# Kernel optimization log

Measured on AMD Instinct MI355X. Metric: run time of the kernel, lower is better.

Reference implementation:

```python
import jax, jax.numpy as jnp
import numpy as np

N_NODES = 50000
N_EDGES = 800000


def setup_inputs() -> dict:
    key = jax.random.key(0)
    ks = jax.random.split(key, 9)
    d, h, hd = 128, 4, 32
    s = 1.0 / np.sqrt(d)
    return {
        "x": jax.random.normal(ks[0], (N_NODES, d), jnp.float32),
        "edge_index": jax.random.randint(ks[1], (2, N_EDGES), 0, N_NODES, jnp.int32),
        "W0": jax.random.normal(ks[2], (d, d), jnp.float32) * s,
        "att_l0": jax.random.normal(ks[3], (h, hd), jnp.float32) * s,
        "att_r0": jax.random.normal(ks[4], (h, hd), jnp.float32) * s,
        "b0": jnp.zeros((d,), jnp.float32),
        "W1": jax.random.normal(ks[5], (d, d), jnp.float32) * s,
        "att_l1": jax.random.normal(ks[6], (h, hd), jnp.float32) * s,
        "att_r1": jax.random.normal(ks[7], (h, hd), jnp.float32) * s,
        "b1": jnp.zeros((hd,), jnp.float32),
    }


def _gat_layer(x, src, dst, W, att_l, att_r, bias, concat):
    # x: [N, F_in]; W: [H*D, F_in] (torch Linear layout); att_*: [H, D]
    n = x.shape[0]
    h, d = att_l.shape
    hx = (x @ W.T).reshape(n, h, d)                     # [N,H,D]
    al = jnp.einsum('nhd,hd->nh', hx, att_l)            # [N,H]
    ar = jnp.einsum('nhd,hd->nh', hx, att_r)
    att = al[src] + ar[dst]                             # [E,H]
    att = jax.nn.leaky_relu(att, negative_slope=0.2)
    # segment softmax over destination nodes
    m = jax.ops.segment_max(att, dst, num_segments=n)   # [N,H]
    att = jnp.exp(att - m[dst])
    ssum = jax.ops.segment_sum(att, dst, num_segments=n)
    att = att / (ssum[dst] + 1e-9)                      # [E,H]
    msgs = att[:, :, None] * hx[src]                    # [E,H,D]
    out = jax.ops.segment_sum(msgs, dst, num_segments=n)  # [N,H,D]
    if concat:
        out = out.reshape(n, h * d)
    else:
        out = out.mean(axis=1)
    return out + bias


def reference(x, edge_index, W0, att_l0, att_r0, b0, W1, att_l1, att_r1, b1):
    src, dst = edge_index[0], edge_index[1]
    x = _gat_layer(x, src, dst, W0, att_l0, att_r0, b0, concat=True)
    x = jax.nn.relu(x)  # dropout is identity in eval mode
    x = _gat_layer(x, src, dst, W1, att_l1, att_r1, b1, concat=False)
    return x
```

## Files before the change

### kernel.cpp

```cpp
#include <hip/hip_runtime.h>
#include <hip/hip_bf16.h>

#define H 4
#define D 32
#define F 128
#define MAXDEG 64
#define PF 16
#define NBUCK 256
#define BUCKW 196
#define CAP   4096

typedef __attribute__((ext_vector_type(8))) short bf16x8;
typedef __attribute__((ext_vector_type(4))) float f32x4;

__device__ __forceinline__ short f2bf(float v) {
    __hip_bfloat16 h = __float2bfloat16(v);
    return *reinterpret_cast<short*>(&h);
}
__device__ __forceinline__ float bf2f(short s) {
    __hip_bfloat16 h = *reinterpret_cast<__hip_bfloat16*>(&s);
    return __bfloat162float(h);
}

__device__ __forceinline__
void gemm_body(int bid, int nblocks, const float* __restrict__ X,
               const float* __restrict__ W, const float* __restrict__ attl,
               const float* __restrict__ attr, __hip_bfloat16* __restrict__ HXB,
               float* __restrict__ AL, float* __restrict__ AR, int ntiles) {
    const int wave = threadIdx.x >> 6;
    const int lane = threadIdx.x & 63;
    const int m    = lane & 15;
    const int q    = lane >> 4;
    const int q8   = q * 8;

    bf16x8 Bhi[2][4], Blo[2][4];
#pragma unroll
    for (int j = 0; j < 2; ++j) {
        const int fout = wave * 32 + j * 16 + m;
#pragma unroll
        for (int kc = 0; kc < 4; ++kc) {
            const float* wp = W + (size_t)fout * F + kc * 32 + q8;
            float4 w0 = *reinterpret_cast<const float4*>(wp);
            float4 w1 = *reinterpret_cast<const float4*>(wp + 4);
            float wv[8] = {w0.x, w0.y, w0.z, w0.w, w1.x, w1.y, w1.z, w1.w};
#pragma unroll
            for (int t = 0; t < 8; ++t) {
                short h = f2bf(wv[t]);
                Bhi[j][kc][t] = h;
                Blo[j][kc][t] = f2bf(wv[t] - bf2f(h));
            }
        }
    }
    const float alw0  = attl[wave * 32 + m];
    const float alw16 = attl[wave * 32 + 16 + m];
    const float arw0  = attr[wave * 32 + m];
    const float arw16 = attr[wave * 32 + 16 + m];

    for (int tile = bid; tile < ntiles; tile += nblocks) {
        const int node0 = tile * 16;
        bf16x8 Ahi[4], Alo[4];
        const float* xp = X + (size_t)(node0 + m) * F + q8;
#pragma unroll
        for (int kc = 0; kc < 4; ++kc) {
            float4 x0 = *reinterpret_cast<const float4*>(xp + kc * 32);
            float4 x1 = *reinterpret_cast<const float4*>(xp + kc * 32 + 4);
            float xv[8] = {x0.x, x0.y, x0.z, x0.w, x1.x, x1.y, x1.z, x1.w};
#pragma unroll
            for (int t = 0; t < 8; ++t) {
                short h = f2bf(xv[t]);
                Ahi[kc][t] = h;
                Alo[kc][t] = f2bf(xv[t] - bf2f(h));
            }
        }
        f32x4 acc0 = {0.f, 0.f, 0.f, 0.f};
        f32x4 acc1 = {0.f, 0.f, 0.f, 0.f};
#pragma unroll
        for (int kc = 0; kc < 4; ++kc) {
            acc0 = __builtin_amdgcn_mfma_f32_16x16x32_bf16(Ahi[kc], Bhi[0][kc], acc0, 0, 0, 0);
            acc1 = __builtin_amdgcn_mfma_f32_16x16x32_bf16(Ahi[kc], Bhi[1][kc], acc1, 0, 0, 0);
            acc0 = __builtin_amdgcn_mfma_f32_16x16x32_bf16(Ahi[kc], Blo[0][kc], acc0, 0, 0, 0);
            acc1 = __builtin_amdgcn_mfma_f32_16x16x32_bf16(Ahi[kc], Blo[1][kc], acc1, 0, 0, 0);
            acc0 = __builtin_amdgcn_mfma_f32_16x16x32_bf16(Alo[kc], Bhi[0][kc], acc0, 0, 0, 0);
            acc1 = __builtin_amdgcn_mfma_f32_16x16x32_bf16(Alo[kc], Bhi[1][kc], acc1, 0, 0, 0);
        }
        const int row0 = node0 + q * 4;
        const int col0 = wave * 32 + m;
#pragma unroll
        for (int r = 0; r < 4; ++r) {
            HXB[(size_t)(row0 + r) * F + col0]      = __float2bfloat16(acc0[r]);
            HXB[(size_t)(row0 + r) * F + col0 + 16] = __float2bfloat16(acc1[r]);
            float pal = acc0[r] * alw0 + acc1[r] * alw16;
            float par = acc0[r] * arw0 + acc1[r] * arw16;
#pragma unroll
            for (int o = 1; o < 16; o <<= 1) {
                pal += __shfl_xor(pal, o);
                par += __shfl_xor(par, o);
            }
            if (m == 0) {
                AL[(size_t)(row0 + r) * H + wave] = pal;
                AR[(size_t)(row0 + r) * H + wave] = par;
            }
        }
    }
}

__device__ __forceinline__
void wconv_body(const float* __restrict__ W1, __hip_bfloat16* __restrict__ W1hi,
                __hip_bfloat16* __restrict__ W1lo) {
    for (int i = threadIdx.x; i < F * F; i += 256) {
        float v = W1[i];
        short hi = f2bf(v);
        *reinterpret_cast<short*>(&W1hi[i]) = hi;
        *reinterpret_cast<short*>(&W1lo[i]) = f2bf(v - bf2f(hi));
    }
}

__device__ __forceinline__
void bucketA_body(int abid, int nablk, const int* __restrict__ ei, int E,
                  int* __restrict__ gcnt, unsigned int* __restrict__ buf) {
    __shared__ int lcnt[NBUCK];
    __shared__ int lpos[NBUCK];
    const int tid = threadIdx.x;
    lcnt[tid] = 0;
    __syncthreads();
    const int per = E / nablk;
    const int e0 = abid * per;
    const int e1 = (abid == nablk - 1) ? E : e0 + per;
    for (int e = e0 + tid; e < e1; e += 256)
        atomicAdd(&lcnt[ei[E + e] / BUCKW], 1);
    __syncthreads();
    if (lcnt[tid] > 0)
        lpos[tid] = atomicAdd(&gcnt[tid], lcnt[tid]);
    __syncthreads();
    for (int e = e0 + tid; e < e1; e += 256) {
        int src = ei[e];
        int dst = ei[E + e];
        int b = dst / BUCKW;
        int pos = atomicAdd(&lpos[b], 1);
        if (pos < CAP)
            buf[(size_t)b * CAP + pos] =
                (unsigned)src | ((unsigned)(dst - b * BUCKW) << 16);
    }
}

__global__ __launch_bounds__(256)
void k_pre(const float* __restrict__ X, const float* __restrict__ W0,
           const float* __restrict__ attl0, const float* __restrict__ attr0,
           __hip_bfloat16* __restrict__ HXB, float* __restrict__ AL,
           float* __restrict__ AR, int ntiles, int gemm_blocks,
           const float* __restrict__ W1, __hip_bfloat16* __restrict__ W1hi,
           __hip_bfloat16* __restrict__ W1lo,
           const int* __restrict__ ei, int E, int nablk,
           int* __restrict__ gcnt, unsigned int* __restrict__ buf) {
    const int bid = blockIdx.x;
    if (bid < gemm_blocks)
        gemm_body(bid, gemm_blocks, X, W0, attl0, attr0, HXB, AL, AR, ntiles);
    else if (bid == gemm_blocks)
        wconv_body(W1, W1hi, W1lo);
    else
        bucketA_body(bid - gemm_blocks - 1, nablk, ei, E, gcnt, buf);
}

__global__ __launch_bounds__(256)
void k_bucket(const unsigned int* __restrict__ buf, const int* __restrict__ gcnt,
              int* __restrict__ deg, unsigned short* __restrict__ ssrc2u, int N) {
    __shared__ int cnt[BUCKW];
    const int b = blockIdx.x;
    const int tid = threadIdx.x;
    if (tid < BUCKW) cnt[tid] = 0;
    __syncthreads();
    const int m = min(gcnt[b], CAP);
    for (int i = tid; i < m; i += 256) {
        unsigned rec = buf[(size_t)b * CAP + i];
        int src  = rec & 0xffff;
        int ldst = rec >> 16;
        int slot = atomicAdd(&cnt[ldst], 1);
        if (slot < MAXDEG)
            ssrc2u[(size_t)(b * BUCKW + ldst) * MAXDEG + slot] = (unsigned short)src;
    }
    __syncthreads();
    if (tid < BUCKW) {
        int node = b * BUCKW + tid;
        if (node < N) deg[node] = cnt[tid];
    }
}

__device__ __forceinline__
int stage_node(int g, int t, int n, const unsigned short* __restrict__ ssrc2u,
               const int* __restrict__ deg, const float* __restrict__ AL,
               const float4 ar4, int (*sidx)[MAXDEG], float (*sw)[MAXDEG][H]) {
    const int cnt  = min(deg[n], MAXDEG);
    const int rcnt = (cnt + PF - 1) & ~(PF - 1);
    if (t < rcnt) {
        if (t < cnt) {
            int s = ssrc2u[n * MAXDEG + t];
            sidx[g][t] = s;
            float4 al4 = *reinterpret_cast<const float4*>(AL + (size_t)s * H);
            float a0 = al4.x + ar4.x; a0 = a0 > 0.f ? a0 : 0.2f * a0;
            float a1 = al4.y + ar4.y; a1 = a1 > 0.f ? a1 : 0.2f * a1;
            float a2 = al4.z + ar4.z; a2 = a2 > 0.f ? a2 : 0.2f * a2;
            float a3 = al4.w + ar4.w; a3 = a3 > 0.f ? a3 : 0.2f * a3;
            sw[g][t][0] = __expf(a0);
            sw[g][t][1] = __expf(a1);
            sw[g][t][2] = __expf(a2);
            sw[g][t][3] = __expf(a3);
        } else {
            sidx[g][t] = 0;
            sw[g][t][0] = 0.f; sw[g][t][1] = 0.f; sw[g][t][2] = 0.f; sw[g][t][3] = 0.f;
        }
    }
    __builtin_amdgcn_wave_barrier();
    return rcnt;
}

__device__ __forceinline__
void gather_node(int g, int t, int h, int rcnt, const __hip_bfloat16* __restrict__ HXB,
                 const int (*sidx)[MAXDEG], const float (*sw)[MAXDEG][H],
                 float& accx, float& accy, float& wsum) {
    for (int base = 0; base < rcnt; base += PF) {
        __hip_bfloat162 v[PF];
#pragma unroll
        for (int j = 0; j < PF; ++j) {
            int s = sidx[g][base + j];
            v[j] = *reinterpret_cast<const __hip_bfloat162*>(HXB + (size_t)s * F + 2 * t);
        }
#pragma unroll
        for (int j = 0; j < PF; ++j) {
            float w = sw[g][base + j][h];
            float2 f = __bfloat1622float2(v[j]);
            accx += w * f.x;
            accy += w * f.y;
            wsum += w;
        }
    }
}

__global__ __launch_bounds__(256)
void k_aggr0(const unsigned short* __restrict__ ssrc2u, const int* __restrict__ deg,
             const float* __restrict__ AL, const float* __restrict__ AR,
             const __hip_bfloat16* __restrict__ HXB, const float* __restrict__ bias,
             float* __restrict__ out, int N) {
    __shared__ int   sidx[4][MAXDEG];
    __shared__ float sw[4][MAXDEG][H];
    const int g = threadIdx.x >> 6;
    const int t = threadIdx.x & 63;
    const int n = blockIdx.x * 4 + g;
    if (n >= N) return;
    const int h = t >> 4;
    const float4 ar4 = *reinterpret_cast<const float4*>(AR + (size_t)n * H);
    int rcnt = stage_node(g, t, n, ssrc2u, deg, AL, ar4, sidx, sw);
    float accx = 0.f, accy = 0.f, wsum = 0.f;
    gather_node(g, t, h, rcnt, HXB, sidx, sw, accx, accy, wsum);
    float inv = 1.f / (wsum + 1e-9f);
    float2 o;
    o.x = fmaxf(accx * inv + bias[2 * t], 0.f);
    o.y = fmaxf(accy * inv + bias[2 * t + 1], 0.f);
    *reinterpret_cast<float2*>(out + (size_t)n * F + 2 * t) = o;
}

__global__ __launch_bounds__(256)
void k_gemm1(const float* __restrict__ X, const __hip_bfloat16* __restrict__ W1hi,
             const __hip_bfloat16* __restrict__ W1lo,
             const float* __restrict__ attl, const float* __restrict__ attr,
             __hip_bfloat16* __restrict__ HXB, float* __restrict__ AL,
             float* __restrict__ AR, int ntiles) {
    const int wave = threadIdx.x >> 6;
    const int lane = threadIdx.x & 63;
    const int m    = lane & 15;
    const int q    = lane >> 4;
    const int q8   = q * 8;

    bf16x8 Bhi[2][4], Blo[2][4];
#pragma unroll
    for (int j = 0; j < 2; ++j) {
        const int fout = wave * 32 + j * 16 + m;
#pragma unroll
        for (int kc = 0; kc < 4; ++kc) {
            Bhi[j][kc] = *reinterpret_cast<const bf16x8*>(W1hi + (size_t)fout * F + kc * 32 + q8);
            Blo[j][kc] = *reinterpret_cast<const bf16x8*>(W1lo + (size_t)fout * F + kc * 32 + q8);
        }
    }
    const float alw0  = attl[wave * 32 + m];
    const float alw16 = attl[wave * 32 + 16 + m];
    const float arw0  = attr[wave * 32 + m];
    const float arw16 = attr[wave * 32 + 16 + m];

    for (int tile = blockIdx.x; tile < ntiles; tile += gridDim.x) {
        const int node0 = tile * 16;
        bf16x8 Ahi[4], Alo[4];
        const float* xp = X + (size_t)(node0 + m) * F + q8;
#pragma unroll
        for (int kc = 0; kc < 4; ++kc) {
            float4 x0 = *reinterpret_cast<const float4*>(xp + kc * 32);
            float4 x1 = *reinterpret_cast<const float4*>(xp + kc * 32 + 4);
            float xv[8] = {x0.x, x0.y, x0.z, x0.w, x1.x, x1.y, x1.z, x1.w};
#pragma unroll
            for (int t = 0; t < 8; ++t) {
                short h = f2bf(xv[t]);
                Ahi[kc][t] = h;
                Alo[kc][t] = f2bf(xv[t] - bf2f(h));
            }
        }
        f32x4 acc0 = {0.f, 0.f, 0.f, 0.f};
        f32x4 acc1 = {0.f, 0.f, 0.f, 0.f};
#pragma unroll
        for (int kc = 0; kc < 4; ++kc) {
            acc0 = __builtin_amdgcn_mfma_f32_16x16x32_bf16(Ahi[kc], Bhi[0][kc], acc0, 0, 0, 0);
            acc1 = __builtin_amdgcn_mfma_f32_16x16x32_bf16(Ahi[kc], Bhi[1][kc], acc1, 0, 0, 0);
            acc0 = __builtin_amdgcn_mfma_f32_16x16x32_bf16(Ahi[kc], Blo[0][kc], acc0, 0, 0, 0);
            acc1 = __builtin_amdgcn_mfma_f32_16x16x32_bf16(Ahi[kc], Blo[1][kc], acc1, 0, 0, 0);
            acc0 = __builtin_amdgcn_mfma_f32_16x16x32_bf16(Alo[kc], Bhi[0][kc], acc0, 0, 0, 0);
            acc1 = __builtin_amdgcn_mfma_f32_16x16x32_bf16(Alo[kc], Bhi[1][kc], acc1, 0, 0, 0);
        }
        const int row0 = node0 + q * 4;
        const int col0 = wave * 32 + m;
#pragma unroll
        for (int r = 0; r < 4; ++r) {
            HXB[(size_t)(row0 + r) * F + col0]      = __float2bfloat16(acc0[r]);
            HXB[(size_t)(row0 + r) * F + col0 + 16] = __float2bfloat16(acc1[r]);
            float pal = acc0[r] * alw0 + acc1[r] * alw16;
            float par = acc0[r] * arw0 + acc1[r] * arw16;
#pragma unroll
            for (int o = 1; o < 16; o <<= 1) {
                pal += __shfl_xor(pal, o);
                par += __shfl_xor(par, o);
            }
            if (m == 0) {
                AL[(size_t)(row0 + r) * H + wave] = pal;
                AR[(size_t)(row0 + r) * H + wave] = par;
            }
        }
    }
}

__global__ __launch_bounds__(256)
void k_aggr1(const unsigned short* __restrict__ ssrc2u, const int* __restrict__ deg,
             const float* __restrict__ AL, const float* __restrict__ AR,
             const __hip_bfloat16* __restrict__ HXB, const float* __restrict__ bias,
             float* __restrict__ out, int N) {
    __shared__ int   sidx[4][MAXDEG];
    __shared__ float sw[4][MAXDEG][H];
    const int g = threadIdx.x >> 6;
    const int t = threadIdx.x & 63;
    const int n = blockIdx.x * 4 + g;
    if (n >= N) return;
    const int h = t >> 4;
    const float4 ar4 = *reinterpret_cast<const float4*>(AR + (size_t)n * H);
    int rcnt = stage_node(g, t, n, ssrc2u, deg, AL, ar4, sidx, sw);
    float accx = 0.f, accy = 0.f, wsum = 0.f;
    gather_node(g, t, h, rcnt, HXB, sidx, sw, accx, accy, wsum);
    float inv = 1.f / (wsum + 1e-9f);
    float vx = accx * inv, vy = accy * inv;
    vx += __shfl_xor(vx, 16); vx += __shfl_xor(vx, 32);
    vy += __shfl_xor(vy, 16); vy += __shfl_xor(vy, 32);
    if (t < 16) {
        float2 o;
        o.x = 0.25f * vx + bias[2 * t];
        o.y = 0.25f * vy + bias[2 * t + 1];
        *reinterpret_cast<float2*>(out + (size_t)n * D + 2 * t) = o;
    }
}

extern "C" void kernel_launch(void* const* d_in, const int* in_sizes, int n_in,
                              void* d_out, int out_size, void* d_ws, size_t ws_size,
                              hipStream_t stream) {
    const float* x     = (const float*)d_in[0];
    const int*   ei    = (const int*)d_in[1];
    const float* W0    = (const float*)d_in[2];
    const float* attl0 = (const float*)d_in[3];
    const float* attr0 = (const float*)d_in[4];
    const float* b0    = (const float*)d_in[5];
    const float* W1    = (const float*)d_in[6];
    const float* attl1 = (const float*)d_in[7];
    const float* attr1 = (const float*)d_in[8];
    const float* b1    = (const float*)d_in[9];

    const int N = in_sizes[0] / F;
    const int E = in_sizes[1] / 2;
    const int ntiles = N / 16;
    const int nablk  = 128;

    char* p = (char*)d_ws;
    __hip_bfloat16* HXB  = (__hip_bfloat16*)p;  p += (size_t)N * F * 2;
    float* X1  = (float*)p;                     p += (size_t)N * F * 4;
    __hip_bfloat16* W1hi = (__hip_bfloat16*)p;  p += (size_t)F * F * 2;
    __hip_bfloat16* W1lo = (__hip_bfloat16*)p;  p += (size_t)F * F * 2;
    float* AL  = (float*)p;                     p += (size_t)N * H * 4;
    float* AR  = (float*)p;                     p += (size_t)N * H * 4;
    unsigned short* ssrc2u = (unsigned short*)p; p += (size_t)N * MAXDEG * 2;
    int* deg = (int*)p;                         p += (size_t)N * 4;
    unsigned int* buf = (unsigned int*)p;       p += (size_t)NBUCK * CAP * 4;
    int* gcnt = (int*)p;

    hipMemsetAsync(gcnt, 0, NBUCK * sizeof(int), stream);

    const int gemm_blocks = 625;

    k_pre<<<gemm_blocks + 1 + nablk, 256, 0, stream>>>(
        x, W0, attl0, attr0, HXB, AL, AR, ntiles, gemm_blocks,
        W1, W1hi, W1lo, ei, E, nablk, gcnt, buf);

    k_bucket<<<NBUCK, 256, 0, stream>>>(buf, gcnt, deg, ssrc2u, N);

    k_aggr0<<<(N + 3) / 4, 256, 0, stream>>>(ssrc2u, deg, AL, AR, HXB, b0, X1, N);

    k_gemm1<<<gemm_blocks, 256, 0, stream>>>(X1, W1hi, W1lo, attl1, attr1,
                                             HXB, AL, AR, ntiles);

    k_aggr1<<<(N + 3) / 4, 256, 0, stream>>>(ssrc2u, deg, AL, AR, HXB, b1,
                                             (float*)d_out, N);
}
```

Measured before the change: 214.8 us.

## Restructure preprocessing: precompute bf16 weight splits, fuse bucket pass with GEMM0, emit bf16 X1

Result: slower. 244.0 us (+13.6%).

```diff
diff --git a/kernel.cpp b/kernel.cpp
--- a/kernel.cpp
+++ b/kernel.cpp
@@ -9,6 +9,7 @@
 #define NBUCK 256
 #define BUCKW 196
 #define CAP   4096
+#define NABLK 128
 
 typedef __attribute__((ext_vector_type(8))) short bf16x8;
 typedef __attribute__((ext_vector_type(4))) float f32x4;
@@ -23,8 +24,116 @@
 }
 
 __device__ __forceinline__
-void gemm_body(int bid, int nblocks, const float* __restrict__ X,
-               const float* __restrict__ W, const float* __restrict__ attl,
+void wconv_body(const float* __restrict__ W, short* __restrict__ Whi,
+                short* __restrict__ Wlo) {
+    for (int i = threadIdx.x * 4; i < F * F; i += 1024) {
+        float4 v = *reinterpret_cast<const float4*>(W + i);
+        float vv[4] = {v.x, v.y, v.z, v.w};
+        short hs[4], ls[4];
+#pragma unroll
+        for (int j = 0; j < 4; ++j) {
+            hs[j] = f2bf(vv[j]);
+            ls[j] = f2bf(vv[j] - bf2f(hs[j]));
+        }
+        *reinterpret_cast<short4*>(Whi + i) = make_short4(hs[0], hs[1], hs[2], hs[3]);
+        *reinterpret_cast<short4*>(Wlo + i) = make_short4(ls[0], ls[1], ls[2], ls[3]);
+    }
+}
+
+__device__ __forceinline__
+void bucketA_body(int abid, const int* __restrict__ ei, int E,
+                  int* __restrict__ gcnt, unsigned int* __restrict__ buf) {
+    __shared__ int lcnt[NBUCK];
+    __shared__ int lpos[NBUCK];
+    const int tid = threadIdx.x;
+    lcnt[tid] = 0;
+    __syncthreads();
+    const int per = ((E / NABLK) + 3) & ~3;
+    const int e0 = abid * per;
+    const int e1 = min(e0 + per, E);
+    for (int e = e0 + 4 * tid; e < e1; e += 1024) {
+        int4 dv = *reinterpret_cast<const int4*>(ei + E + e);
+        atomicAdd(&lcnt[dv.x / BUCKW], 1);
+        atomicAdd(&lcnt[dv.y / BUCKW], 1);
+        atomicAdd(&lcnt[dv.z / BUCKW], 1);
+        atomicAdd(&lcnt[dv.w / BUCKW], 1);
+    }
+    __syncthreads();
+    if (lcnt[tid] > 0)
+        lpos[tid] = atomicAdd(&gcnt[tid], lcnt[tid]);
+    __syncthreads();
+    for (int e = e0 + 4 * tid; e < e1; e += 1024) {
+        int4 sv = *reinterpret_cast<const int4*>(ei + e);
+        int4 dv = *reinterpret_cast<const int4*>(ei + E + e);
+        int ss[4] = {sv.x, sv.y, sv.z, sv.w};
+        int dd[4] = {dv.x, dv.y, dv.z, dv.w};
+#pragma unroll
+        for (int j = 0; j < 4; ++j) {
+            int b = dd[j] / BUCKW;
+            int pos = atomicAdd(&lpos[b], 1);
+            if (pos < CAP)
+                buf[(size_t)b * CAP + pos] =
+                    (unsigned)ss[j] | ((unsigned)(dd[j] - b * BUCKW) << 16);
+        }
+    }
+}
+
+__global__ __launch_bounds__(256)
+void k_prep(const float* __restrict__ W0, short* __restrict__ W0hi,
+            short* __restrict__ W0lo, const float* __restrict__ W1,
+            short* __restrict__ W1hi, short* __restrict__ W1lo,
+            const int* __restrict__ ei, int E,
+            int* __restrict__ gcnt, unsigned int* __restrict__ buf) {
+    if (blockIdx.x < NABLK)
+        bucketA_body(blockIdx.x, ei, E, gcnt, buf);
+    else if (blockIdx.x == NABLK)
+        wconv_body(W0, W0hi, W0lo);
+    else
+        wconv_body(W1, W1hi, W1lo);
+}
+
+__device__ __forceinline__
+void bucketB_body(int b, const unsigned int* __restrict__ buf,
+                  const int* __restrict__ gcnt, int* __restrict__ deg,
+                  unsigned short* __restrict__ ssrc2u, int N) {
+    __shared__ int cnt[BUCKW];
+    const int tid = threadIdx.x;
+    if (tid < BUCKW) cnt[tid] = 0;
+    __syncthreads();
+    const int mm = min(gcnt[b], CAP);
+    const int m4 = mm & ~3;
+    for (int i = 4 * tid; i < m4; i += 1024) {
+        uint4 r = *reinterpret_cast<const uint4*>(buf + (size_t)b * CAP + i);
+        unsigned rr[4] = {r.x, r.y, r.z, r.w};
+#pragma unroll
+        for (int j = 0; j < 4; ++j) {
+            int src  = rr[j] & 0xffff;
+            int ldst = rr[j] >> 16;
+            int slot = atomicAdd(&cnt[ldst], 1);
+            if (slot < MAXDEG)
+                ssrc2u[(size_t)(b * BUCKW + ldst) * MAXDEG + slot] = (unsigned short)src;
+        }
+    }
+    for (int i = m4 + tid; i < mm; i += 256) {
+        unsigned rec = buf[(size_t)b * CAP + i];
+        int src  = rec & 0xffff;
+        int ldst = rec >> 16;
+        int slot = atomicAdd(&cnt[ldst], 1);
+        if (slot < MAXDEG)
+            ssrc2u[(size_t)(b * BUCKW + ldst) * MAXDEG + slot] = (unsigned short)src;
+    }
+    __syncthreads();
+    if (tid < BUCKW) {
+        int node = b * BUCKW + tid;
+        if (node < N) deg[node] = cnt[tid];
+    }
+}
+
+template<bool AFP32>
+__device__ __forceinline__
+void gemm_core(int bid, int nblocks, const void* __restrict__ Xv,
+               const short* __restrict__ Xlo_, const short* __restrict__ Whi,
+               const short* __restrict__ Wlo, const float* __restrict__ attl,
                const float* __restrict__ attr, __hip_bfloat16* __restrict__ HXB,
                float* __restrict__ AL, float* __restrict__ AR, int ntiles) {
     const int wave = threadIdx.x >> 6;
@@ -39,16 +148,8 @@
         const int fout = wave * 32 + j * 16 + m;
 #pragma unroll
         for (int kc = 0; kc < 4; ++kc) {
-            const float* wp = W + (size_t)fout * F + kc * 32 + q8;
-            float4 w0 = *reinterpret_cast<const float4*>(wp);
-            float4 w1 = *reinterpret_cast<const float4*>(wp + 4);
-            float wv[8] = {w0.x, w0.y, w0.z, w0.w, w1.x, w1.y, w1.z, w1.w};
-#pragma unroll
-            for (int t = 0; t < 8; ++t) {
-                short h = f2bf(wv[t]);
-                Bhi[j][kc][t] = h;
-                Blo[j][kc][t] = f2bf(wv[t] - bf2f(h));
-            }
+            Bhi[j][kc] = *reinterpret_cast<const bf16x8*>(Whi + (size_t)fout * F + kc * 32 + q8);
+            Blo[j][kc] = *reinterpret_cast<const bf16x8*>(Wlo + (size_t)fout * F + kc * 32 + q8);
         }
     }
     const float alw0  = attl[wave * 32 + m];
@@ -59,17 +160,27 @@
     for (int tile = bid; tile < ntiles; tile += nblocks) {
         const int node0 = tile * 16;
         bf16x8 Ahi[4], Alo[4];
-        const float* xp = X + (size_t)(node0 + m) * F + q8;
-#pragma unroll
-        for (int kc = 0; kc < 4; ++kc) {
-            float4 x0 = *reinterpret_cast<const float4*>(xp + kc * 32);
-            float4 x1 = *reinterpret_cast<const float4*>(xp + kc * 32 + 4);
-            float xv[8] = {x0.x, x0.y, x0.z, x0.w, x1.x, x1.y, x1.z, x1.w};
-#pragma unroll
-            for (int t = 0; t < 8; ++t) {
-                short h = f2bf(xv[t]);
-                Ahi[kc][t] = h;
-                Alo[kc][t] = f2bf(xv[t] - bf2f(h));
+        if constexpr (AFP32) {
+            const float* xp = reinterpret_cast<const float*>(Xv) + (size_t)(node0 + m) * F + q8;
+#pragma unroll
+            for (int kc = 0; kc < 4; ++kc) {
+                float4 x0 = *reinterpret_cast<const float4*>(xp + kc * 32);
+                float4 x1 = *reinterpret_cast<const float4*>(xp + kc * 32 + 4);
+                float xv[8] = {x0.x, x0.y, x0.z, x0.w, x1.x, x1.y, x1.z, x1.w};
+#pragma unroll
+                for (int t = 0; t < 8; ++t) {
+                    short h = f2bf(xv[t]);
+                    Ahi[kc][t] = h;
+                    Alo[kc][t] = f2bf(xv[t] - bf2f(h));
+                }
+            }
+        } else {
+            const short* xh = reinterpret_cast<const short*>(Xv) + (size_t)(node0 + m) * F + q8;
+            const short* xl = Xlo_ + (size_t)(node0 + m) * F + q8;
+#pragma unroll
+            for (int kc = 0; kc < 4; ++kc) {
+                Ahi[kc] = *reinterpret_cast<const bf16x8*>(xh + kc * 32);
+                Alo[kc] = *reinterpret_cast<const bf16x8*>(xl + kc * 32);
             }
         }
         f32x4 acc0 = {0.f, 0.f, 0.f, 0.f};
@@ -104,85 +215,28 @@
     }
 }
 
-__device__ __forceinline__
-void wconv_body(const float* __restrict__ W1, __hip_bfloat16* __restrict__ W1hi,
-                __hip_bfloat16* __restrict__ W1lo) {
-    for (int i = threadIdx.x; i < F * F; i += 256) {
-        float v = W1[i];
-        short hi = f2bf(v);
-        *reinterpret_cast<short*>(&W1hi[i]) = hi;
-        *reinterpret_cast<short*>(&W1lo[i]) = f2bf(v - bf2f(hi));
-    }
-}
-
-__device__ __forceinline__
-void bucketA_body(int abid, int nablk, const int* __restrict__ ei, int E,
-                  int* __restrict__ gcnt, unsigned int* __restrict__ buf) {
-    __shared__ int lcnt[NBUCK];
-    __shared__ int lpos[NBUCK];
-    const int tid = threadIdx.x;
-    lcnt[tid] = 0;
-    __syncthreads();
-    const int per = E / nablk;
-    const int e0 = abid * per;
-    const int e1 = (abid == nablk - 1) ? E : e0 + per;
-    for (int e = e0 + tid; e < e1; e += 256)
-        atomicAdd(&lcnt[ei[E + e] / BUCKW], 1);
-    __syncthreads();
-    if (lcnt[tid] > 0)
-        lpos[tid] = atomicAdd(&gcnt[tid], lcnt[tid]);
-    __syncthreads();
-    for (int e = e0 + tid; e < e1; e += 256) {
-        int src = ei[e];
-        int dst = ei[E + e];
-        int b = dst / BUCKW;
-        int pos = atomicAdd(&lpos[b], 1);
-        if (pos < CAP)
-            buf[(size_t)b * CAP + pos] =
-                (unsigned)src | ((unsigned)(dst - b * BUCKW) << 16);
-    }
-}
-
-__global__ __launch_bounds__(256)
-void k_pre(const float* __restrict__ X, const float* __restrict__ W0,
-           const float* __restrict__ attl0, const float* __restrict__ attr0,
-           __hip_bfloat16* __restrict__ HXB, float* __restrict__ AL,
-           float* __restrict__ AR, int ntiles, int gemm_blocks,
-           const float* __restrict__ W1, __hip_bfloat16* __restrict__ W1hi,
-           __hip_bfloat16* __restrict__ W1lo,
-           const int* __restrict__ ei, int E, int nablk,
-           int* __restrict__ gcnt, unsigned int* __restrict__ buf) {
-    const int bid = blockIdx.x;
-    if (bid < gemm_blocks)
-        gemm_body(bid, gemm_blocks, X, W0, attl0, attr0, HXB, AL, AR, ntiles);
-    else if (bid == gemm_blocks)
-        wconv_body(W1, W1hi, W1lo);
+__global__ __launch_bounds__(256)
+void k_g0(const unsigned int* __restrict__ buf, const int* __restrict__ gcnt,
+          int* __restrict__ deg, unsigned short* __restrict__ ssrc2u, int N,
+          const float* __restrict__ X, const short* __restrict__ W0hi,
+          const short* __restrict__ W0lo, const float* __restrict__ attl0,
+          const float* __restrict__ attr0, __hip_bfloat16* __restrict__ HXB,
+          float* __restrict__ AL, float* __restrict__ AR, int ntiles) {
+    if (blockIdx.x < NBUCK)
+        bucketB_body(blockIdx.x, buf, gcnt, deg, ssrc2u, N);
     else
-        bucketA_body(bid - gemm_blocks - 1, nablk, ei, E, gcnt, buf);
-}
-
-__global__ __launch_bounds__(256)
-void k_bucket(const unsigned int* __restrict__ buf, const int* __restrict__ gcnt,
-              int* __restrict__ deg, unsigned short* __restrict__ ssrc2u, int N) {
-    __shared__ int cnt[BUCKW];
-    const int b = blockIdx.x;
-    const int tid = threadIdx.x;
-    if (tid < BUCKW) cnt[tid] = 0;
-    __syncthreads();
-    const int m = min(gcnt[b], CAP);
-    for (int i = tid; i < m; i += 256) {
-        unsigned rec = buf[(size_t)b * CAP + i];
-        int src  = rec & 0xffff;
-        int ldst = rec >> 16;
-        int slot = atomicAdd(&cnt[ldst], 1);
-        if (slot < MAXDEG)
-            ssrc2u[(size_t)(b * BUCKW + ldst) * MAXDEG + slot] = (unsigned short)src;
-    }
-    __syncthreads();
-    if (tid < BUCKW) {
-        int node = b * BUCKW + tid;
-        if (node < N) deg[node] = cnt[tid];
-    }
+        gemm_core<true>(blockIdx.x - NBUCK, gridDim.x - NBUCK, X, nullptr,
+                        W0hi, W0lo, attl0, attr0, HXB, AL, AR, ntiles);
+}
+
+__global__ __launch_bounds__(256)
+void k_gemm1(const short* __restrict__ X1hi, const short* __restrict__ X1lo,
+             const short* __restrict__ W1hi, const short* __restrict__ W1lo,
+             const float* __restrict__ attl, const float* __restrict__ attr,
+             __hip_bfloat16* __restrict__ HXB, float* __restrict__ AL,
+             float* __restrict__ AR, int ntiles) {
+    gemm_core<false>(blockIdx.x, gridDim.x, X1hi, X1lo, W1hi, W1lo,
+                     attl, attr, HXB, AL, AR, ntiles);
 }
 
 __device__ __forceinline__
@@ -239,7 +293,7 @@
 void k_aggr0(const unsigned short* __restrict__ ssrc2u, const int* __restrict__ deg,
              const float* __restrict__ AL, const float* __restrict__ AR,
              const __hip_bfloat16* __restrict__ HXB, const float* __restrict__ bias,
-             float* __restrict__ out, int N) {
+             short* __restrict__ X1hi, short* __restrict__ X1lo, int N) {
     __shared__ int   sidx[4][MAXDEG];
     __shared__ float sw[4][MAXDEG][H];
     const int g = threadIdx.x >> 6;
@@ -252,85 +306,14 @@
     float accx = 0.f, accy = 0.f, wsum = 0.f;
     gather_node(g, t, h, rcnt, HXB, sidx, sw, accx, accy, wsum);
     float inv = 1.f / (wsum + 1e-9f);
-    float2 o;
-    o.x = fmaxf(accx * inv + bias[2 * t], 0.f);
-    o.y = fmaxf(accy * inv + bias[2 * t + 1], 0.f);
-    *reinterpret_cast<float2*>(out + (size_t)n * F + 2 * t) = o;
-}
-
-__global__ __launch_bounds__(256)
-void k_gemm1(const float* __restrict__ X, const __hip_bfloat16* __restrict__ W1hi,
-             const __hip_bfloat16* __restrict__ W1lo,
-             const float* __restrict__ attl, const float* __restrict__ attr,
-             __hip_bfloat16* __restrict__ HXB, float* __restrict__ AL,
-             float* __restrict__ AR, int ntiles) {
-    const int wave = threadIdx.x >> 6;
-    const int lane = threadIdx.x & 63;
-    const int m    = lane & 15;
-    const int q    = lane >> 4;
-    const int q8   = q * 8;
-
-    bf16x8 Bhi[2][4], Blo[2][4];
-#pragma unroll
-    for (int j = 0; j < 2; ++j) {
-        const int fout = wave * 32 + j * 16 + m;
-#pragma unroll
-        for (int kc = 0; kc < 4; ++kc) {
-            Bhi[j][kc] = *reinterpret_cast<const bf16x8*>(W1hi + (size_t)fout * F + kc * 32 + q8);
-            Blo[j][kc] = *reinterpret_cast<const bf16x8*>(W1lo + (size_t)fout * F + kc * 32 + q8);
-        }
-    }
-    const float alw0  = attl[wave * 32 + m];
-    const float alw16 = attl[wave * 32 + 16 + m];
-    const float arw0  = attr[wave * 32 + m];
-    const float arw16 = attr[wave * 32 + 16 + m];
-
-    for (int tile = blockIdx.x; tile < ntiles; tile += gridDim.x) {
-        const int node0 = tile * 16;
-        bf16x8 Ahi[4], Alo[4];
-        const float* xp = X + (size_t)(node0 + m) * F + q8;
-#pragma unroll
-        for (int kc = 0; kc < 4; ++kc) {
-            float4 x0 = *reinterpret_cast<const float4*>(xp + kc * 32);
-            float4 x1 = *reinterpret_cast<const float4*>(xp + kc * 32 + 4);
-            float xv[8] = {x0.x, x0.y, x0.z, x0.w, x1.x, x1.y, x1.z, x1.w};
-#pragma unroll
-            for (int t = 0; t < 8; ++t) {
-                short h = f2bf(xv[t]);
-                Ahi[kc][t] = h;
-                Alo[kc][t] = f2bf(xv[t] - bf2f(h));
-            }
-        }
-        f32x4 acc0 = {0.f, 0.f, 0.f, 0.f};
-        f32x4 acc1 = {0.f, 0.f, 0.f, 0.f};
-#pragma unroll
-        for (int kc = 0; kc < 4; ++kc) {
-            acc0 = __builtin_amdgcn_mfma_f32_16x16x32_bf16(Ahi[kc], Bhi[0][kc], acc0, 0, 0, 0);
-            acc1 = __builtin_amdgcn_mfma_f32_16x16x32_bf16(Ahi[kc], Bhi[1][kc], acc1, 0, 0, 0);
-            acc0 = __builtin_amdgcn_mfma_f32_16x16x32_bf16(Ahi[kc], Blo[0][kc], acc0, 0, 0, 0);
-            acc1 = __builtin_amdgcn_mfma_f32_16x16x32_bf16(Ahi[kc], Blo[1][kc], acc1, 0, 0, 0);
-            acc0 = __builtin_amdgcn_mfma_f32_16x16x32_bf16(Alo[kc], Bhi[0][kc], acc0, 0, 0, 0);
-            acc1 = __builtin_amdgcn_mfma_f32_16x16x32_bf16(Alo[kc], Bhi[1][kc], acc1, 0, 0, 0);
-        }
-        const int row0 = node0 + q * 4;
-        const int col0 = wave * 32 + m;
-#pragma unroll
-        for (int r = 0; r < 4; ++r) {
-            HXB[(size_t)(row0 + r) * F + col0]      = __float2bfloat16(acc0[r]);
-            HXB[(size_t)(row0 + r) * F + col0 + 16] = __float2bfloat16(acc1[r]);
-            float pal = acc0[r] * alw0 + acc1[r] * alw16;
-            float par = acc0[r] * arw0 + acc1[r] * arw16;
-#pragma unroll
-            for (int o = 1; o < 16; o <<= 1) {
-                pal += __shfl_xor(pal, o);
-                par += __shfl_xor(par, o);
-            }
-            if (m == 0) {
-                AL[(size_t)(row0 + r) * H + wave] = pal;
-                AR[(size_t)(row0 + r) * H + wave] = par;
-            }
-        }
-    }
+    float ox = fmaxf(accx * inv + bias[2 * t], 0.f);
+    float oy = fmaxf(accy * inv + bias[2 * t + 1], 0.f);
+    short h0 = f2bf(ox), h1 = f2bf(oy);
+    short l0 = f2bf(ox - bf2f(h0)), l1 = f2bf(oy - bf2f(h1));
+    unsigned hw = (unsigned)(unsigned short)h0 | ((unsigned)(unsigned short)h1 << 16);
+    unsigned lw = (unsigned)(unsigned short)l0 | ((unsigned)(unsigned short)l1 << 16);
+    *reinterpret_cast<unsigned*>(X1hi + (size_t)n * F + 2 * t) = hw;
+    *reinterpret_cast<unsigned*>(X1lo + (size_t)n * F + 2 * t) = lw;
 }
 
 __global__ __launch_bounds__(256)
@@ -378,15 +361,17 @@
     const int N = in_sizes[0] / F;
     const int E = in_sizes[1] / 2;
     const int ntiles = N / 16;
-    const int nablk  = 128;
 
     char* p = (char*)d_ws;
-    __hip_bfloat16* HXB  = (__hip_bfloat16*)p;  p += (size_t)N * F * 2;
-    float* X1  = (float*)p;                     p += (size_t)N * F * 4;
-    __hip_bfloat16* W1hi = (__hip_bfloat16*)p;  p += (size_t)F * F * 2;
-    __hip_bfloat16* W1lo = (__hip_bfloat16*)p;  p += (size_t)F * F * 2;
-    float* AL  = (float*)p;                     p += (size_t)N * H * 4;
-    float* AR  = (float*)p;                     p += (size_t)N * H * 4;
+    __hip_bfloat16* HXB = (__hip_bfloat16*)p;   p += (size_t)N * F * 2;
+    short* X1hi = (short*)p;                    p += (size_t)N * F * 2;
+    short* X1lo = (short*)p;                    p += (size_t)N * F * 2;
+    short* W0hi = (short*)p;                    p += (size_t)F * F * 2;
+    short* W0lo = (short*)p;                    p += (size_t)F * F * 2;
+    short* W1hi = (short*)p;                    p += (size_t)F * F * 2;
+    short* W1lo = (short*)p;                    p += (size_t)F * F * 2;
+    float* AL   = (float*)p;                    p += (size_t)N * H * 4;
+    float* AR   = (float*)p;                    p += (size_t)N * H * 4;
     unsigned short* ssrc2u = (unsigned short*)p; p += (size_t)N * MAXDEG * 2;
     int* deg = (int*)p;                         p += (size_t)N * 4;
     unsigned int* buf = (unsigned int*)p;       p += (size_t)NBUCK * CAP * 4;
@@ -394,18 +379,18 @@
 
     hipMemsetAsync(gcnt, 0, NBUCK * sizeof(int), stream);
 
-    const int gemm_blocks = 625;
-
-    k_pre<<<gemm_blocks + 1 + nablk, 256, 0, stream>>>(
-        x, W0, attl0, attr0, HXB, AL, AR, ntiles, gemm_blocks,
-        W1, W1hi, W1lo, ei, E, nablk, gcnt, buf);
-
-    k_bucket<<<NBUCK, 256, 0, stream>>>(buf, gcnt, deg, ssrc2u, N);
-
-    k_aggr0<<<(N + 3) / 4, 256, 0, stream>>>(ssrc2u, deg, AL, AR, HXB, b0, X1, N);
-
-    k_gemm1<<<gemm_blocks, 256, 0, stream>>>(X1, W1hi, W1lo, attl1, attr1,
+    k_prep<<<NABLK + 2, 256, 0, stream>>>(W0, W0hi, W0lo, W1, W1hi, W1lo,
+                                          ei, E, gcnt, buf);
+
+    k_g0<<<NBUCK + ntiles, 256, 0, stream>>>(buf, gcnt, deg, ssrc2u, N,
+                                             x, W0hi, W0lo, attl0, attr0,
                                              HXB, AL, AR, ntiles);
+
+    k_aggr0<<<(N + 3) / 4, 256, 0, stream>>>(ssrc2u, deg, AL, AR, HXB, b0,
+                                             X1hi, X1lo, N);
+
+    k_gemm1<<<ntiles, 256, 0, stream>>>(X1hi, X1lo, W1hi, W1lo, attl1, attr1,
+                                        HXB, AL, AR, ntiles);
 
     k_aggr1<<<(N + 3) / 4, 256, 0, stream>>>(ssrc2u, deg, AL, AR, HXB, b1,
                                              (float*)d_out, N);
```
